# Performance work log

Hardware: AMD Instinct MI355X
Metric: run time of the kernel (lower is better)

Reference implementation:

```python
import jax, jax.numpy as jnp
import numpy as np

MID = 16
HEADS = 8
HEAD_DIM = MID // HEADS  # 2
EPS = 1e-5


def posembed(length, dim):
    # get_posembed_linear: sin-cos 1D positional embedding
    pos = jnp.arange(length, dtype=jnp.float32)
    omega = jnp.arange(dim // 2, dtype=jnp.float32) / (dim / 2.0)
    omega = 1.0 / (10000.0 ** omega)
    out = pos[:, None] * omega[None, :]  # [L, dim//2]
    return jnp.concatenate([jnp.sin(out), jnp.cos(out)], axis=1)  # [L, dim]


def layernorm(x, g, b):
    m = x.mean(-1, keepdims=True)
    v = ((x - m) ** 2).mean(-1, keepdims=True)
    return (x - m) * jax.lax.rsqrt(v + EPS) * g + b


def conv2d(x, w, b):
    # NCHW 3x3 SAME conv
    y = jax.lax.conv_general_dilated(x, w, (1, 1), 'SAME',
                                     dimension_numbers=('NCHW', 'OIHW', 'NCHW'))
    return y + b[None, :, None, None]


def attention(x, wq, wk, wv, wo, bo):
    # diffusers Attention: self-attn, no qkv bias, out bias
    B, S, C = x.shape
    q = (x @ wq.T).reshape(B, S, HEADS, HEAD_DIM)
    k = (x @ wk.T).reshape(B, S, HEADS, HEAD_DIM)
    v = (x @ wv.T).reshape(B, S, HEADS, HEAD_DIM)
    scale = 1.0 / np.sqrt(HEAD_DIM).astype(np.float32)
    scores = jnp.einsum('bshd,bthd->bhst', q, k) * scale
    p = jax.nn.softmax(scores, axis=-1)
    o = jnp.einsum('bhst,bthd->bshd', p, v).reshape(B, S, C)
    return o @ wo.T + bo


def setup_inputs() -> dict:
    key = jax.random.key(0)
    ks = jax.random.split(key, 24)

    def n(k, shape, s=0.05):
        return jax.random.normal(k, shape, dtype=jnp.float32) * s

    b, f, h, w, c = 2, 16, 64, 64, 16
    inp = {
        'hidden_states': n(ks[0], (b, f, h, w, c), 1.0),
        'ref_stats': n(ks[1], (b, f, h, w, c), 1.0),
        'emb': n(ks[2], (b, 512), 1.0),
        'conv_in_w': n(ks[3], (MID, c, 3, 3)),
        'conv_in_b': jnp.zeros((MID,), jnp.float32),
        'emb1_w': n(ks[4], (MID, 512)),
        'emb1_b': jnp.zeros((MID,), jnp.float32),
        'emb2_w': n(ks[5], (MID, MID)),
        'emb2_b': jnp.zeros((MID,), jnp.float32),
        'wqx': n(ks[6], (MID, MID)), 'wkx': n(ks[7], (MID, MID)),
        'wvx': n(ks[8], (MID, MID)), 'wox': n(ks[9], (MID, MID)),
        'box': jnp.zeros((MID,), jnp.float32),
        'wqy': n(ks[10], (MID, MID)), 'wky': n(ks[11], (MID, MID)),
        'wvy': n(ks[12], (MID, MID)), 'woy': n(ks[13], (MID, MID)),
        'boy': jnp.zeros((MID,), jnp.float32),
        'wqt': n(ks[14], (MID, MID)), 'wkt': n(ks[15], (MID, MID)),
        'wvt': n(ks[16], (MID, MID)), 'wot': n(ks[17], (MID, MID)),
        'bot': jnp.zeros((MID,), jnp.float32),
        'norm_g': jnp.ones((MID,), jnp.float32),
        'norm_b': jnp.zeros((MID,), jnp.float32),
        'proj_w': n(ks[18], (c, MID, 3, 3)),  # zero_module in torch; random here so grads flow
        'proj_b': jnp.zeros((c,), jnp.float32),
    }
    return inp


def reference(hidden_states, ref_stats, emb,
              conv_in_w, conv_in_b, emb1_w, emb1_b, emb2_w, emb2_b,
              wqx, wkx, wvx, wox, box,
              wqy, wky, wvy, woy, boy,
              wqt, wkt, wvt, wot, bot,
              norm_g, norm_b, proj_w, proj_b):
    b, f, h, w, c = hidden_states.shape

    # conv stem on (b f) c h w
    x = hidden_states.reshape(b * f, h, w, c).transpose(0, 3, 1, 2)
    x = conv2d(x, conv_in_w, conv_in_b)
    r = ref_stats.reshape(b * f, h, w, c).transpose(0, 3, 1, 2)
    r = conv2d(r, conv_in_w, conv_in_b)

    # TimestepEmbedding: linear -> silu -> linear, broadcast over frames/HW
    e = jax.nn.silu(emb @ emb1_w.T + emb1_b) @ emb2_w.T + emb2_b  # [b, MID]
    r = r + jnp.repeat(e, f, axis=0)[:, :, None, None]

    hs = x.reshape(b, f, MID, h, w).transpose(0, 1, 3, 4, 2)  # b f h w c
    rs = r.reshape(b, f, MID, h, w).transpose(0, 1, 3, 4, 2)

    # row (x) attention: cat along w -> (b f h) 2w c
    cat = jnp.concatenate([hs, rs], axis=3).reshape(b * f * h, 2 * w, MID)
    pe = posembed(2 * w, MID)
    resx = attention(layernorm(cat + pe[None], norm_g, norm_b), wqx, wkx, wvx, wox, box)
    resx = resx[:, :w].reshape(b, f, h, w, MID)

    # column (y) attention: cat along h -> (b f w) 2h c
    cat = jnp.concatenate([resx, rs], axis=2)            # b f 2h w c
    cat = cat.transpose(0, 1, 3, 2, 4).reshape(b * f * w, 2 * h, MID)
    pe = posembed(2 * h, MID)
    resy = attention(layernorm(cat + pe[None], norm_g, norm_b), wqy, wky, wvy, woy, boy)
    resy = resy[:, :h].reshape(b, f, w, h, MID).transpose(0, 1, 3, 2, 4)

    # temporal (t) attention: cat along f -> (b h w) 2f c
    cat = jnp.concatenate([resy, rs], axis=1)            # b 2f h w c
    cat = cat.transpose(0, 2, 3, 1, 4).reshape(b * h * w, 2 * f, MID)
    pe = posembed(2 * f, MID)
    rest = attention(layernorm(cat + pe[None], norm_g, norm_b), wqt, wkt, wvt, wot, bot)
    rest = rest[:, :f].reshape(b, h, w, f, MID).transpose(0, 3, 4, 1, 2).reshape(b * f, MID, h, w)

    out = conv2d(rest, proj_w, proj_b)  # (b f) c h w
    return hidden_states + out.reshape(b, f, c, h, w).transpose(0, 1, 3, 4, 2)
```

## Files before the change

kernel.cpp:

```cpp
#include <hip/hip_runtime.h>
#include <hip/hip_bf16.h>

typedef __hip_bfloat16 bf16;

__device__ __forceinline__ float b2f(bf16 x) { return __bfloat162float(x); }

#define BB   2
#define FF   16
#define HH   64
#define WW   64
#define CC   16
#define NIMG (BB*FF)
#define PIX  (HH*WW)
#define IMGSZ (PIX*CC)

#define QSCALE_LOG2E 1.0201394f

__device__ __forceinline__ void ld16bf(const bf16* p, float* x) {
    const uint4* p4 = reinterpret_cast<const uint4*>(p);
    uint4 u0 = p4[0], u1 = p4[1];
    unsigned uu[8] = {u0.x, u0.y, u0.z, u0.w, u1.x, u1.y, u1.z, u1.w};
    #pragma unroll
    for (int k = 0; k < 8; ++k) {
        union { unsigned u; float f; } lo, hi;
        lo.u = uu[k] << 16;
        hi.u = uu[k] & 0xffff0000u;
        x[2 * k] = lo.f;
        x[2 * k + 1] = hi.f;
    }
}
__device__ __forceinline__ void st16bf(bf16* p, const float* x) {
    union { bf16 h[16]; uint4 u[2]; } o;
    #pragma unroll
    for (int k = 0; k < 16; ++k) o.h[k] = __float2bfloat16(x[k]);
    uint4* p4 = reinterpret_cast<uint4*>(p);
    p4[0] = o.u[0];
    p4[1] = o.u[1];
}

__device__ __forceinline__ void ld16f(const float* p, float* x) {
    const float4* p4 = reinterpret_cast<const float4*>(p);
    #pragma unroll
    for (int q = 0; q < 4; ++q) {
        float4 v = p4[q];
        x[4 * q] = v.x; x[4 * q + 1] = v.y; x[4 * q + 2] = v.z; x[4 * q + 3] = v.w;
    }
}
__device__ __forceinline__ void st16f(float* p, const float* x) {
    float4* p4 = reinterpret_cast<float4*>(p);
    #pragma unroll
    for (int q = 0; q < 4; ++q)
        p4[q] = make_float4(x[4 * q], x[4 * q + 1], x[4 * q + 2], x[4 * q + 3]);
}

__device__ __forceinline__ unsigned packbf2(float a, float b) {
    union { bf16 h[2]; unsigned u; } pk;
    pk.h[0] = __float2bfloat16(a);
    pk.h[1] = __float2bfloat16(b);
    return pk.u;
}

__global__ __launch_bounds__(256) void conv_in_kernel(
    const float* __restrict__ hid, const float* __restrict__ ref,
    const float* __restrict__ cw, const float* __restrict__ cb,
    const float* __restrict__ emb,
    const float* __restrict__ e1w, const float* __restrict__ e1b,
    const float* __restrict__ e2w, const float* __restrict__ e2b,
    bf16* __restrict__ A, bf16* __restrict__ R)
{
    __shared__ float wl[9 * 256];
    __shared__ float bl[16];
    __shared__ float hl[16];
    __shared__ float el[16];
    int t = threadIdx.x;
    {
        int ic = t >> 4, oc = t & 15;
        #pragma unroll
        for (int k = 0; k < 9; ++k)
            wl[k * 256 + t] = cw[(oc * 16 + ic) * 9 + k];
    }
    if (t < 16) bl[t] = cb[t];

    int gid  = blockIdx.x * 256 + t;
    int wi   = gid & 63;
    int hi   = (gid >> 6) & 63;
    int img2 = gid >> 12;
    int isref = img2 >> 5;
    int img  = img2 & 31;
    int bi   = img >> 4;

    if (isref) {
        if (t < 16) {
            float acc = e1b[t];
            const float* er = emb + bi * 512;
            const float* wr = e1w + t * 512;
            for (int k = 0; k < 512; ++k) acc = fmaf(er[k], wr[k], acc);
            hl[t] = acc / (1.f + __expf(-acc));
        }
        __syncthreads();
        if (t < 16) {
            float acc = e2b[t];
            #pragma unroll
            for (int k = 0; k < 16; ++k) acc = fmaf(hl[k], e2w[t * 16 + k], acc);
            el[t] = acc;
        }
    }
    __syncthreads();

    const float* inp = (isref ? ref : hid) + (size_t)img * IMGSZ;
    float acc[16];
    #pragma unroll
    for (int oc = 0; oc < 16; ++oc)
        acc[oc] = bl[oc] + (isref ? el[oc] : 0.f);

    for (int ky = 0; ky < 3; ++ky) {
        int y = hi + ky - 1;
        if ((unsigned)y >= 64u) continue;
        for (int kx = 0; kx < 3; ++kx) {
            int x = wi + kx - 1;
            if ((unsigned)x >= 64u) continue;
            float xv[16];
            ld16f(inp + (((y << 6) + x) << 4), xv);
            const float* wt = &wl[(ky * 3 + kx) * 256];
            #pragma unroll
            for (int ic = 0; ic < 16; ++ic) {
                #pragma unroll
                for (int oc = 0; oc < 16; ++oc)
                    acc[oc] = fmaf(xv[ic], wt[ic * 16 + oc], acc[oc]);
            }
        }
    }
    bf16* op = (isref ? R : A) + ((size_t)(img * PIX + (hi << 6) + wi) << 4);
    st16bf(op, acc);
}

template<int S, int SEQPB, int MINW>
__global__ __launch_bounds__(256, MINW) void attn_kernel(
    bf16* __restrict__ A, const bf16* __restrict__ R,
    int d2, int str1, int str2, int tokStride,
    const float* __restrict__ wq, const float* __restrict__ wk,
    const float* __restrict__ wv, const float* __restrict__ wo,
    const float* __restrict__ bo, const float* __restrict__ gw,
    const float* __restrict__ bw)
{
    constexpr int HS  = S / 2;
    constexpr int KQ  = S / 2;
    constexpr int TPT = 256 / (SEQPB * S);
    constexpr int ITEMS = 256 / SEQPB;
    constexpr int NQG = ITEMS / 16;
    constexpr int QB  = HS / NQG;
    constexpr int KROW = 10;
    constexpr int QROW = 20;
    constexpr int LSQ = (SEQPB == 1) ? 0 : ((SEQPB == 2) ? 1 : 2);
    constexpr int NW3 = SEQPB * HS * 8 / 256;

    __shared__ float wql[256], wkl[256], wvl[256], wolT[256];
    __shared__ float bol[16], gl[16], blw[16];
    __shared__ __align__(16) unsigned kU[SEQPB * S * KROW];
    __shared__ __align__(16) unsigned vU[SEQPB * S * KROW];
    __shared__ __align__(16) float qoL[SEQPB * HS * QROW];
    __shared__ int bases[SEQPB];

    int t = threadIdx.x;
    wql[t] = wq[t] * QSCALE_LOG2E;
    wkl[t] = wk[t];
    wvl[t] = wv[t];
    wolT[(t & 15) * 16 + (t >> 4)] = wo[t];
    if (t < 16) { bol[t] = bo[t]; gl[t] = gw[t]; blw[t] = bw[t]; }
    if (t < SEQPB) {
        int seq = blockIdx.x * SEQPB + t;
        bases[t] = (seq / d2) * str1 + (seq % d2) * str2;
    }
    __syncthreads();

    {
        int tokIdx, sq, i, db, ndim;
        if (TPT == 2) {
            tokIdx = t >> 1;
            db = (t & 1) * 8;
            ndim = 8;
        } else {
            tokIdx = t;
            db = 0;
            ndim = 16;
        }
        sq = tokIdx & (SEQPB - 1);
        i  = tokIdx >> LSQ;
        const bf16* src = (i < HS)
            ? (A + bases[sq] + (size_t)i * tokStride)
            : (R + bases[sq] + (size_t)(i - HS) * tokStride);
        float x[16];
        ld16bf(src, x);
        const float om[8] = {1.f, 0.31622776601683794f, 0.1f, 0.031622776601683794f,
                             0.01f, 0.0031622776601683794f, 0.001f, 0.00031622776601683794f};
        float fi = (float)i;
        #pragma unroll
        for (int k = 0; k < 8; ++k) {
            float sv, cv;
            __sincosf(fi * om[k], &sv, &cv);
            x[k]     += sv;
            x[k + 8] += cv;
        }
        float m = 0.f;
        #pragma unroll
        for (int c = 0; c < 16; ++c) m += x[c];
        m *= (1.f / 16.f);
        float var = 0.f;
        #pragma unroll
        for (int c = 0; c < 16; ++c) { float d = x[c] - m; var = fmaf(d, d, var); }
        var *= (1.f / 16.f);
        float rs = rsqrtf(var + 1e-5f);
        float xn[16];
        #pragma unroll
        for (int c = 0; c < 16; ++c) xn[c] = (x[c] - m) * rs * gl[c] + blw[c];

        float qv[16], kv[16], vv[16];
        #pragma unroll
        for (int dd = 0; dd < 16; ++dd) {
            if (dd >= ndim) break;
            int d = db + dd;
            float aq = 0.f, ak = 0.f, av = 0.f;
            #pragma unroll
            for (int c = 0; c < 16; ++c) {
                aq = fmaf(xn[c], wql[d * 16 + c], aq);
                ak = fmaf(xn[c], wkl[d * 16 + c], ak);
                av = fmaf(xn[c], wvl[d * 16 + c], av);
            }
            qv[dd] = aq; kv[dd] = ak; vv[dd] = av;
        }
        int row = (sq * S + i) * KROW + (db >> 1);
        uint2* kr = reinterpret_cast<uint2*>(&kU[row]);
        uint2* vr = reinterpret_cast<uint2*>(&vU[row]);
        #pragma unroll
        for (int e = 0; e < ndim / 4; ++e) {
            kr[e] = make_uint2(packbf2(kv[4 * e], kv[4 * e + 1]),
                               packbf2(kv[4 * e + 2], kv[4 * e + 3]));
            vr[e] = make_uint2(packbf2(vv[4 * e], vv[4 * e + 1]),
                               packbf2(vv[4 * e + 2], vv[4 * e + 3]));
        }
        if (i < HS) {
            float* qrow = &qoL[(sq * HS + i) * QROW + db];
            #pragma unroll
            for (int e = 0; e < ndim / 4; ++e)
                reinterpret_cast<float4*>(qrow)[e] =
                    make_float4(qv[4 * e], qv[4 * e + 1], qv[4 * e + 2], qv[4 * e + 3]);
        }
    }
    __syncthreads();

    int sq2 = t / ITEMS;
    int r   = t % ITEMS;
    int qg  = r >> 4;
    int hd  = (r >> 1) & 7;
    int half = r & 1;
    {
        float q0[QB], q1[QB], l[QB], a0[QB], a1[QB];
        #pragma unroll
        for (int qq = 0; qq < QB; ++qq) {
            float2 qv = *reinterpret_cast<const float2*>(
                &qoL[(sq2 * HS + qg * QB + qq) * QROW + 2 * hd]);
            q0[qq] = qv.x;
            q1[qq] = qv.y;
            l[qq] = 0.f; a0[qq] = 0.f; a1[qq] = 0.f;
        }
        const unsigned* kp = &kU[(sq2 * S + half) * KROW + hd];
        const unsigned* vp = &vU[(sq2 * S + half) * KROW + hd];
        #pragma unroll 8
        for (int jj = 0; jj < KQ; ++jj) {
            unsigned ku = kp[jj * 2 * KROW];
            unsigned vu = vp[jj * 2 * KROW];
            union { unsigned u; float f; } k0, k1, v0, v1;
            k0.u = ku << 16; k1.u = ku & 0xffff0000u;
            v0.u = vu << 16; v1.u = vu & 0xffff0000u;
            #pragma unroll
            for (int qq = 0; qq < QB; ++qq) {
                float s = fmaf(q0[qq], k0.f, q1[qq] * k1.f);
                float p = __builtin_amdgcn_exp2f(s);
                l[qq] += p;
                a0[qq] = fmaf(p, v0.f, a0[qq]);
                a1[qq] = fmaf(p, v1.f, a1[qq]);
            }
        }
        #pragma unroll
        for (int qq = 0; qq < QB; ++qq) {
            l[qq]  += __shfl_xor(l[qq], 1);
            a0[qq] += __shfl_xor(a0[qq], 1);
            a1[qq] += __shfl_xor(a1[qq], 1);
        }
        __syncthreads();
        if (half == 0) {
            #pragma unroll
            for (int qq = 0; qq < QB; ++qq) {
                float inv = 1.f / l[qq];
                *reinterpret_cast<float2*>(
                    &qoL[(sq2 * HS + qg * QB + qq) * QROW + 2 * hd]) =
                    make_float2(a0[qq] * inv, a1[qq] * inv);
            }
        }
    }
    __syncthreads();

    #pragma unroll
    for (int rep = 0; rep < NW3; ++rep) {
        int idx = t + rep * 256;
        int cp  = idx & 7;
        int g   = idx >> 3;
        int sq3 = g & (SEQPB - 1);
        int tok = g >> LSQ;
        const float* orow = &qoL[(sq3 * HS + tok) * QROW];
        float acc0 = bol[2 * cp], acc1 = bol[2 * cp + 1];
        #pragma unroll
        for (int d = 0; d < 16; ++d) {
            acc0 = fmaf(orow[d], wolT[d * 16 + 2 * cp], acc0);
            acc1 = fmaf(orow[d], wolT[d * 16 + 2 * cp + 1], acc1);
        }
        *reinterpret_cast<unsigned*>(
            A + bases[sq3] + (size_t)tok * tokStride + 2 * cp) =
            packbf2(acc0, acc1);
    }
}

__global__ __launch_bounds__(256) void conv_out_kernel(
    const bf16* __restrict__ A, const float* __restrict__ hid,
    const float* __restrict__ pw, const float* __restrict__ pb,
    float* __restrict__ out)
{
    __shared__ float wl[9 * 256];
    __shared__ float bl[16];
    int t = threadIdx.x;
    {
        int ic = t >> 4, oc = t & 15;
        #pragma unroll
        for (int k = 0; k < 9; ++k)
            wl[k * 256 + t] = pw[(oc * 16 + ic) * 9 + k];
    }
    if (t < 16) bl[t] = pb[t];
    __syncthreads();

    int gid = blockIdx.x * 256 + t;
    int wi = gid & 63, hi = (gid >> 6) & 63;
    int img = gid >> 12;
    const bf16* inp = A + ((size_t)img << 16);
    float acc[16];
    #pragma unroll
    for (int oc = 0; oc < 16; ++oc) acc[oc] = bl[oc];

    for (int ky = 0; ky < 3; ++ky) {
        int y = hi + ky - 1;
        if ((unsigned)y >= 64u) continue;
        for (int kx = 0; kx < 3; ++kx) {
            int x = wi + kx - 1;
            if ((unsigned)x >= 64u) continue;
            float xv[16];
            ld16bf(inp + (((y << 6) + x) << 4), xv);
            const float* wt = &wl[(ky * 3 + kx) * 256];
            #pragma unroll
            for (int ic = 0; ic < 16; ++ic) {
                #pragma unroll
                for (int oc = 0; oc < 16; ++oc)
                    acc[oc] = fmaf(xv[ic], wt[ic * 16 + oc], acc[oc]);
            }
        }
    }
    size_t off = ((size_t)gid) << 4;
    float hv[16];
    ld16f(hid + off, hv);
    float res[16];
    #pragma unroll
    for (int k = 0; k < 16; ++k) res[k] = acc[k] + hv[k];
    st16f(out + off, res);
}

extern "C" void kernel_launch(void* const* d_in, const int* in_sizes, int n_in,
                              void* d_out, int out_size, void* d_ws, size_t ws_size,
                              hipStream_t stream) {
    const float* hid  = (const float*)d_in[0];
    const float* ref  = (const float*)d_in[1];
    const float* emb  = (const float*)d_in[2];
    const float* ciw  = (const float*)d_in[3];
    const float* cib  = (const float*)d_in[4];
    const float* e1w  = (const float*)d_in[5];
    const float* e1b  = (const float*)d_in[6];
    const float* e2w  = (const float*)d_in[7];
    const float* e2b  = (const float*)d_in[8];
    const float* wqx  = (const float*)d_in[9];
    const float* wkx  = (const float*)d_in[10];
    const float* wvx  = (const float*)d_in[11];
    const float* wox  = (const float*)d_in[12];
    const float* box_ = (const float*)d_in[13];
    const float* wqy  = (const float*)d_in[14];
    const float* wky  = (const float*)d_in[15];
    const float* wvy  = (const float*)d_in[16];
    const float* woy  = (const float*)d_in[17];
    const float* boy  = (const float*)d_in[18];
    const float* wqt  = (const float*)d_in[19];
    const float* wkt  = (const float*)d_in[20];
    const float* wvt  = (const float*)d_in[21];
    const float* wot  = (const float*)d_in[22];
    const float* bot  = (const float*)d_in[23];
    const float* ng   = (const float*)d_in[24];
    const float* nb   = (const float*)d_in[25];
    const float* pjw  = (const float*)d_in[26];
    const float* pjb  = (const float*)d_in[27];

    bf16* A = (bf16*)d_ws;
    bf16* R = (bf16*)d_out;

    conv_in_kernel<<<(2 * NIMG * PIX) / 256, 256, 0, stream>>>(
        hid, ref, ciw, cib, emb, e1w, e1b, e2w, e2b, A, R);

    attn_kernel<128, 1, 8><<<BB * FF * HH, 256, 0, stream>>>(
        A, R, 1, WW * CC, 0, CC, wqx, wkx, wvx, wox, box_, ng, nb);
    attn_kernel<128, 2, 4><<<(BB * FF * WW) / 2, 256, 0, stream>>>(
        A, R, WW, IMGSZ, CC, WW * CC, wqy, wky, wvy, woy, boy, ng, nb);
    attn_kernel<32, 4, 8><<<(BB * HH * WW) / 4, 256, 0, stream>>>(
        A, R, HH * WW, FF * IMGSZ, CC, IMGSZ, wqt, wkt, wvt, wot, bot, ng, nb);

    conv_out_kernel<<<(NIMG * PIX) / 256, 256, 0, stream>>>(A, hid, pjw, pjb, (float*)d_out);
}
```

Before: 274.3 us.

## Store K/V as fp32 key-pairs in shared memory and widen y-attention block

K and V are now kept in shared memory as fp32, with two keys interleaved per row so that each thread reads four floats (two keys for one head) with a single float4 load. This replaces the bf16 packing and unpacking. The y-axis attention launch moves to 512 threads for two sequences, so every launch uses a uniform two-threads-per-token projection. Minimum-waves launch bounds change to 6. The fp32 storage doubles K/V shared memory per block, which could lower occupancy, in exchange for wider loads and no bf16 conversion in the inner loop.

```diff
diff --git a/kernel.cpp b/kernel.cpp
--- a/kernel.cpp
+++ b/kernel.cpp
@@ -134,8 +134,8 @@
     st16bf(op, acc);
 }
 
-template<int S, int SEQPB, int MINW>
-__global__ __launch_bounds__(256, MINW) void attn_kernel(
+template<int S, int SEQPB, int NT, int MINW>
+__global__ __launch_bounds__(NT, MINW) void attn_kernel(
     bf16* __restrict__ A, const bf16* __restrict__ R,
     int d2, int str1, int str2, int tokStride,
     const float* __restrict__ wq, const float* __restrict__ wk,
@@ -144,28 +144,30 @@
     const float* __restrict__ bw)
 {
     constexpr int HS  = S / 2;
-    constexpr int KQ  = S / 2;
-    constexpr int TPT = 256 / (SEQPB * S);
-    constexpr int ITEMS = 256 / SEQPB;
+    constexpr int NP  = S / 2;
+    constexpr int PPT = NP / 2;
+    constexpr int ITEMS = NT / SEQPB;
     constexpr int NQG = ITEMS / 16;
     constexpr int QB  = HS / NQG;
-    constexpr int KROW = 10;
+    constexpr int PROW = 36;
     constexpr int QROW = 20;
     constexpr int LSQ = (SEQPB == 1) ? 0 : ((SEQPB == 2) ? 1 : 2);
-    constexpr int NW3 = SEQPB * HS * 8 / 256;
+    constexpr int NW3 = SEQPB * HS * 8 / NT;
 
     __shared__ float wql[256], wkl[256], wvl[256], wolT[256];
     __shared__ float bol[16], gl[16], blw[16];
-    __shared__ __align__(16) unsigned kU[SEQPB * S * KROW];
-    __shared__ __align__(16) unsigned vU[SEQPB * S * KROW];
+    __shared__ __align__(16) float kL[SEQPB * NP * PROW];
+    __shared__ __align__(16) float vL[SEQPB * NP * PROW];
     __shared__ __align__(16) float qoL[SEQPB * HS * QROW];
     __shared__ int bases[SEQPB];
 
     int t = threadIdx.x;
-    wql[t] = wq[t] * QSCALE_LOG2E;
-    wkl[t] = wk[t];
-    wvl[t] = wv[t];
-    wolT[(t & 15) * 16 + (t >> 4)] = wo[t];
+    if (t < 256) {
+        wql[t] = wq[t] * QSCALE_LOG2E;
+        wkl[t] = wk[t];
+        wvl[t] = wv[t];
+        wolT[(t & 15) * 16 + (t >> 4)] = wo[t];
+    }
     if (t < 16) { bol[t] = bo[t]; gl[t] = gw[t]; blw[t] = bw[t]; }
     if (t < SEQPB) {
         int seq = blockIdx.x * SEQPB + t;
@@ -174,18 +176,9 @@
     __syncthreads();
 
     {
-        int tokIdx, sq, i, db, ndim;
-        if (TPT == 2) {
-            tokIdx = t >> 1;
-            db = (t & 1) * 8;
-            ndim = 8;
-        } else {
-            tokIdx = t;
-            db = 0;
-            ndim = 16;
-        }
-        sq = tokIdx & (SEQPB - 1);
-        i  = tokIdx >> LSQ;
+        int tokIdx = t >> 1, halfT = t & 1;
+        int sq = tokIdx & (SEQPB - 1);
+        int i  = tokIdx >> LSQ;
         const bf16* src = (i < HS)
             ? (A + bases[sq] + (size_t)i * tokStride)
             : (R + bases[sq] + (size_t)(i - HS) * tokStride);
@@ -214,10 +207,10 @@
         #pragma unroll
         for (int c = 0; c < 16; ++c) xn[c] = (x[c] - m) * rs * gl[c] + blw[c];
 
-        float qv[16], kv[16], vv[16];
-        #pragma unroll
-        for (int dd = 0; dd < 16; ++dd) {
-            if (dd >= ndim) break;
+        int db = halfT * 8;
+        float qv[8], kv[8], vv[8];
+        #pragma unroll
+        for (int dd = 0; dd < 8; ++dd) {
             int d = db + dd;
             float aq = 0.f, ak = 0.f, av = 0.f;
             #pragma unroll
@@ -228,31 +221,28 @@
             }
             qv[dd] = aq; kv[dd] = ak; vv[dd] = av;
         }
-        int row = (sq * S + i) * KROW + (db >> 1);
-        uint2* kr = reinterpret_cast<uint2*>(&kU[row]);
-        uint2* vr = reinterpret_cast<uint2*>(&vU[row]);
-        #pragma unroll
-        for (int e = 0; e < ndim / 4; ++e) {
-            kr[e] = make_uint2(packbf2(kv[4 * e], kv[4 * e + 1]),
-                               packbf2(kv[4 * e + 2], kv[4 * e + 3]));
-            vr[e] = make_uint2(packbf2(vv[4 * e], vv[4 * e + 1]),
-                               packbf2(vv[4 * e + 2], vv[4 * e + 3]));
+        int p = i >> 1, par = i & 1;
+        float* kr = &kL[(sq * NP + p) * PROW + 2 * par];
+        float* vr = &vL[(sq * NP + p) * PROW + 2 * par];
+        #pragma unroll
+        for (int e = 0; e < 4; ++e) {
+            int hh = 4 * halfT + e;
+            *reinterpret_cast<float2*>(kr + 4 * hh) = make_float2(kv[2 * e], kv[2 * e + 1]);
+            *reinterpret_cast<float2*>(vr + 4 * hh) = make_float2(vv[2 * e], vv[2 * e + 1]);
         }
         if (i < HS) {
             float* qrow = &qoL[(sq * HS + i) * QROW + db];
-            #pragma unroll
-            for (int e = 0; e < ndim / 4; ++e)
-                reinterpret_cast<float4*>(qrow)[e] =
-                    make_float4(qv[4 * e], qv[4 * e + 1], qv[4 * e + 2], qv[4 * e + 3]);
+            reinterpret_cast<float4*>(qrow)[0] = make_float4(qv[0], qv[1], qv[2], qv[3]);
+            reinterpret_cast<float4*>(qrow)[1] = make_float4(qv[4], qv[5], qv[6], qv[7]);
         }
     }
     __syncthreads();
 
     int sq2 = t / ITEMS;
     int r   = t % ITEMS;
+    int kq  = r & 1;
+    int hd  = (r >> 1) & 7;
     int qg  = r >> 4;
-    int hd  = (r >> 1) & 7;
-    int half = r & 1;
     {
         float q0[QB], q1[QB], l[QB], a0[QB], a1[QB];
         #pragma unroll
@@ -263,22 +253,24 @@
             q1[qq] = qv.y;
             l[qq] = 0.f; a0[qq] = 0.f; a1[qq] = 0.f;
         }
-        const unsigned* kp = &kU[(sq2 * S + half) * KROW + hd];
-        const unsigned* vp = &vU[(sq2 * S + half) * KROW + hd];
+        const float* kp = &kL[(sq2 * NP + kq) * PROW + 4 * hd];
+        const float* vp = &vL[(sq2 * NP + kq) * PROW + 4 * hd];
         #pragma unroll 8
-        for (int jj = 0; jj < KQ; ++jj) {
-            unsigned ku = kp[jj * 2 * KROW];
-            unsigned vu = vp[jj * 2 * KROW];
-            union { unsigned u; float f; } k0, k1, v0, v1;
-            k0.u = ku << 16; k1.u = ku & 0xffff0000u;
-            v0.u = vu << 16; v1.u = vu & 0xffff0000u;
+        for (int it = 0; it < PPT; ++it) {
+            float4 kk = *reinterpret_cast<const float4*>(kp + it * 2 * PROW);
+            float4 vv = *reinterpret_cast<const float4*>(vp + it * 2 * PROW);
             #pragma unroll
             for (int qq = 0; qq < QB; ++qq) {
-                float s = fmaf(q0[qq], k0.f, q1[qq] * k1.f);
-                float p = __builtin_amdgcn_exp2f(s);
-                l[qq] += p;
-                a0[qq] = fmaf(p, v0.f, a0[qq]);
-                a1[qq] = fmaf(p, v1.f, a1[qq]);
+                float s0 = fmaf(q0[qq], kk.x, q1[qq] * kk.y);
+                float s1 = fmaf(q0[qq], kk.z, q1[qq] * kk.w);
+                float p0 = __builtin_amdgcn_exp2f(s0);
+                float p1 = __builtin_amdgcn_exp2f(s1);
+                l[qq] += p0;
+                l[qq] += p1;
+                a0[qq] = fmaf(p0, vv.x, a0[qq]);
+                a0[qq] = fmaf(p1, vv.z, a0[qq]);
+                a1[qq] = fmaf(p0, vv.y, a1[qq]);
+                a1[qq] = fmaf(p1, vv.w, a1[qq]);
             }
         }
         #pragma unroll
@@ -288,7 +280,7 @@
             a1[qq] += __shfl_xor(a1[qq], 1);
         }
         __syncthreads();
-        if (half == 0) {
+        if (kq == 0) {
             #pragma unroll
             for (int qq = 0; qq < QB; ++qq) {
                 float inv = 1.f / l[qq];
@@ -302,7 +294,7 @@
 
     #pragma unroll
     for (int rep = 0; rep < NW3; ++rep) {
-        int idx = t + rep * 256;
+        int idx = t + rep * NT;
         int cp  = idx & 7;
         int g   = idx >> 3;
         int sq3 = g & (SEQPB - 1);
@@ -409,11 +401,11 @@
     conv_in_kernel<<<(2 * NIMG * PIX) / 256, 256, 0, stream>>>(
         hid, ref, ciw, cib, emb, e1w, e1b, e2w, e2b, A, R);
 
-    attn_kernel<128, 1, 8><<<BB * FF * HH, 256, 0, stream>>>(
+    attn_kernel<128, 1, 256, 6><<<BB * FF * HH, 256, 0, stream>>>(
         A, R, 1, WW * CC, 0, CC, wqx, wkx, wvx, wox, box_, ng, nb);
-    attn_kernel<128, 2, 4><<<(BB * FF * WW) / 2, 256, 0, stream>>>(
+    attn_kernel<128, 2, 512, 6><<<(BB * FF * WW) / 2, 512, 0, stream>>>(
         A, R, WW, IMGSZ, CC, WW * CC, wqy, wky, wvy, woy, boy, ng, nb);
-    attn_kernel<32, 4, 8><<<(BB * HH * WW) / 4, 256, 0, stream>>>(
+    attn_kernel<32, 4, 256, 6><<<(BB * HH * WW) / 4, 256, 0, stream>>>(
         A, R, HH * WW, FF * IMGSZ, CC, IMGSZ, wqt, wkt, wvt, wot, bot, ng, nb);
 
     conv_out_kernel<<<(NIMG * PIX) / 256, 256, 0, stream>>>(A, hid, pjw, pjb, (float*)d_out);
```

Result: slower. 280.3 us (+2.2%).
